# Kernel tuning notes

Hardware: AMD Instinct MI355X
Metric: run time of the kernel (lower is better)

## Reference

```python
import jax, jax.numpy as jnp
import numpy as np

B, H, N, D = 2, 16, 2048, 128

def setup_inputs() -> dict:
    key = jax.random.key(0)
    kq, kk, kv = jax.random.split(key, 3)
    q = jax.random.normal(kq, (B, H, N, D), dtype=jnp.float32)
    k = jax.random.normal(kk, (B, H, N, D), dtype=jnp.float32)
    v = jax.random.normal(kv, (B, H, N, D), dtype=jnp.float32)
    return {"q": q, "k": k, "v": v}

def reference(q, k, v):
    # scale = 1/sqrt(d) computed at forward time (scale=None in __init__)
    d = q.shape[-1]
    scale = 1.0 / jnp.sqrt(jnp.asarray(d, dtype=q.dtype))
    # scores: (B, H, N, N)
    scores = jnp.einsum('bhnd,bhmd->bhnm', q, k) * scale
    probs = jax.nn.softmax(scores, axis=-1)
    return jnp.einsum('bhnm,bhmd->bhnd', probs, v)
```

## Files before the change

### kernel.cpp

```cpp
#include <hip/hip_runtime.h>
#include <hip/hip_fp16.h>

#define BH   32
#define SEQ  2048
#define DIM  128
#define CK   32
#define NCH  (SEQ / CK)

typedef _Float16 half8   __attribute__((ext_vector_type(8)));
typedef __fp16   fp16x2  __attribute__((ext_vector_type(2)));
typedef _Float16 half2v  __attribute__((ext_vector_type(2)));
typedef float    floatx4 __attribute__((ext_vector_type(4)));

__device__ inline half2v pk2(float a, float b) {
    fp16x2 t = __builtin_amdgcn_cvt_pkrtz(a, b);
    return *(half2v*)&t;
}
__device__ inline half8 pk8(float4 a, float4 b) {
    half2v l0 = pk2(a.x, a.y), l1 = pk2(a.z, a.w);
    half2v l2 = pk2(b.x, b.y), l3 = pk2(b.z, b.w);
    half8 h;
    h[0] = l0[0]; h[1] = l0[1]; h[2] = l1[0]; h[3] = l1[1];
    h[4] = l2[0]; h[5] = l2[1]; h[6] = l3[0]; h[7] = l3[1];
    return h;
}

__device__ inline void ld16(const void* g, void* l) {
    __builtin_amdgcn_global_load_lds(
        (__attribute__((address_space(1))) void*)(uintptr_t)g,
        (__attribute__((address_space(3))) void*)(uintptr_t)l, 16, 0, 0);
}

__device__ inline void wait_vm0() {
    __builtin_amdgcn_s_waitcnt(0x0F70);
}

__global__ void prep_kernel(const float* __restrict__ k, const float* __restrict__ v,
                            _Float16* __restrict__ kh, _Float16* __restrict__ vt) {
    const float SC = 0.08838834764831845f * 1.4426950408889634f;
    __shared__ __align__(16) _Float16 t[32][136];
    const int bh = blockIdx.x >> 6;
    const int kc = blockIdx.x & 63;
    const int tid = threadIdx.x;
    const size_t base = ((size_t)bh * SEQ + kc * CK) * DIM;

    const float4* kf4 = (const float4*)(k + base);
    const float4* vf4 = (const float4*)(v + base);
    half8* kh8 = (half8*)(kh + base);

    #pragma unroll
    for (int i = 0; i < 2; i++) {
        int f8 = i * 256 + tid;
        float4 a = kf4[2 * f8], b = kf4[2 * f8 + 1];
        a.x *= SC; a.y *= SC; a.z *= SC; a.w *= SC;
        b.x *= SC; b.y *= SC; b.z *= SC; b.w *= SC;
        kh8[f8] = pk8(a, b);
        int row = f8 >> 4, c8 = f8 & 15;
        *((half8*)&t[row][c8 * 8]) = pk8(vf4[2 * f8], vf4[2 * f8 + 1]);
    }
    __syncthreads();
    _Float16* vout = vt + ((size_t)bh * NCH + kc) * (DIM * CK);
    #pragma unroll
    for (int i = 0; i < 2; i++) {
        int g = i * 256 + tid;
        int d = g >> 2, kg = g & 3;
        half8 h;
        #pragma unroll
        for (int j = 0; j < 8; j++) h[j] = t[kg * 8 + j][d];
        *((half8*)(vout + d * CK + kg * 8)) = h;
    }
}

__global__ __launch_bounds__(256, 2) void attn_kernel(
        const float* __restrict__ q, const _Float16* __restrict__ kh,
        const _Float16* __restrict__ vt, float* __restrict__ out) {
    __shared__ __align__(16) _Float16 Kbuf[2][CK * DIM];
    __shared__ __align__(16) _Float16 Vbuf[2][DIM * CK];
    __shared__ __align__(16) _Float16 Pld[4][2][16][40];

    const int bh   = blockIdx.y;
    const int qt   = blockIdx.x;
    const int tid  = threadIdx.x;
    const int w    = tid >> 6;
    const int lane = tid & 63;
    const int l15  = lane & 15;
    const int quad = lane >> 4;

    half8 qf[2][4];
    #pragma unroll
    for (int s = 0; s < 2; s++) {
        const float* qb = q + ((size_t)bh * SEQ + qt * 128 + w * 32 + s * 16 + l15) * DIM;
        #pragma unroll
        for (int c = 0; c < 4; c++) {
            float4 a = *((const float4*)(qb + c * 32 + quad * 8));
            float4 b = *((const float4*)(qb + c * 32 + quad * 8 + 4));
            qf[s][c] = pk8(a, b);
        }
    }

    half8 ones;
    #pragma unroll
    for (int j = 0; j < 8; j++) ones[j] = (_Float16)1.0f;

    floatx4 zf = {0.f, 0.f, 0.f, 0.f};
    floatx4 O[2][8];
    #pragma unroll
    for (int s = 0; s < 2; s++)
        #pragma unroll
        for (int i = 0; i < 8; i++) O[s][i] = zf;
    floatx4 Osum[2] = {zf, zf};

    const _Float16* kb = kh + (size_t)bh * SEQ * DIM;
    const _Float16* vb = vt + (size_t)bh * SEQ * DIM;

    const int s0 = w * 128 + lane;
    const int s1 = s0 + 64;
    const int kr0 = s0 >> 4, kg0 = ((s0 & 15) - kr0) & 15;
    const int kr1 = s1 >> 4, kg1 = ((s1 & 15) - kr1) & 15;
    const _Float16* kgp0 = kb + kr0 * DIM + kg0 * 8;
    const _Float16* kgp1 = kb + kr1 * DIM + kg1 * 8;
    const _Float16* vgp0 = vb + s0 * 8;
    const _Float16* vgp1 = vb + s1 * 8;

    auto dma = [&](int kc, int b) {
        size_t off = (size_t)kc * (CK * DIM);
        ld16(kgp0 + off, &Kbuf[b][(w * 2 + 0) * 512]);
        ld16(kgp1 + off, &Kbuf[b][(w * 2 + 1) * 512]);
        ld16(vgp0 + off, &Vbuf[b][(w * 2 + 0) * 512]);
        ld16(vgp1 + off, &Vbuf[b][(w * 2 + 1) * 512]);
    };

    dma(0, 0);

    const int row0 = 2 * l15, row1 = 2 * l15 + 1;

    #pragma unroll 2
    for (int kc = 0; kc < NCH; kc++) {
        wait_vm0();
        __syncthreads();
        if (kc + 1 < NCH) dma(kc + 1, (kc + 1) & 1);

        const _Float16* Kc = Kbuf[kc & 1];
        const _Float16* Vc = Vbuf[kc & 1];

        floatx4 S[2][2];
        #pragma unroll
        for (int s = 0; s < 2; s++) { S[s][0] = zf; S[s][1] = zf; }
        #pragma unroll
        for (int c = 0; c < 4; c++) {
            int g = c * 4 + quad;
            half8 b0 = *((const half8*)&Kc[row0 * DIM + (((g + row0) & 15) * 8)]);
            half8 b1 = *((const half8*)&Kc[row1 * DIM + (((g + row1) & 15) * 8)]);
            #pragma unroll
            for (int s = 0; s < 2; s++) {
                S[s][0] = __builtin_amdgcn_mfma_f32_16x16x32_f16(qf[s][c], b0, S[s][0], 0, 0, 0);
                S[s][1] = __builtin_amdgcn_mfma_f32_16x16x32_f16(qf[s][c], b1, S[s][1], 0, 0, 0);
            }
        }

        #pragma unroll
        for (int s = 0; s < 2; s++)
            #pragma unroll
            for (int r = 0; r < 4; r++) {
                float p0 = exp2f(S[s][0][r]);
                float p1 = exp2f(S[s][1][r]);
                *((half2v*)&Pld[w][s][quad * 4 + r][2 * l15]) = pk2(p0, p1);
            }

        half8 pf0 = *((const half8*)&Pld[w][0][l15][quad * 8]);
        half8 pf1 = *((const half8*)&Pld[w][1][l15][quad * 8]);

        Osum[0] = __builtin_amdgcn_mfma_f32_16x16x32_f16(pf0, ones, Osum[0], 0, 0, 0);
        Osum[1] = __builtin_amdgcn_mfma_f32_16x16x32_f16(pf1, ones, Osum[1], 0, 0, 0);

        #pragma unroll
        for (int dt = 0; dt < 8; dt++) {
            half8 vf = *((const half8*)&Vc[(dt * 16 + l15) * CK + quad * 8]);
            O[0][dt] = __builtin_amdgcn_mfma_f32_16x16x32_f16(pf0, vf, O[0][dt], 0, 0, 0);
            O[1][dt] = __builtin_amdgcn_mfma_f32_16x16x32_f16(pf1, vf, O[1][dt], 0, 0, 0);
        }
    }

    #pragma unroll
    for (int s = 0; s < 2; s++) {
        float* ob = out + ((size_t)bh * SEQ + qt * 128 + w * 32 + s * 16) * DIM;
        #pragma unroll
        for (int r = 0; r < 4; r++) {
            float rinv = 1.0f / Osum[s][r];
            #pragma unroll
            for (int dt = 0; dt < 8; dt++) {
                ob[(size_t)(quad * 4 + r) * DIM + dt * 16 + l15] = O[s][dt][r] * rinv;
            }
        }
    }
}

extern "C" void kernel_launch(void* const* d_in, const int* in_sizes, int n_in,
                              void* d_out, int out_size, void* d_ws, size_t ws_size,
                              hipStream_t stream) {
    const float* q = (const float*)d_in[0];
    const float* k = (const float*)d_in[1];
    const float* v = (const float*)d_in[2];
    float* out = (float*)d_out;

    const size_t elems = (size_t)BH * SEQ * DIM;
    _Float16* kh = (_Float16*)d_ws;
    _Float16* vtp = kh + elems;

    prep_kernel<<<BH * NCH, 256, 0, stream>>>(k, v, kh, vtp);
    attn_kernel<<<dim3(SEQ / 128, BH), 256, 0, stream>>>(q, kh, vtp, out);
}
```

Measured before the change: 212.0 us.

## Triple-buffer K/V DMA with prefetch distance two and XCD-aware block remap

Widens the K/V LDS ring from two to three buffers and issues DMA two chunks ahead. The wait becomes a partial vmcnt(4) plus a single barrier, so the next chunk's loads stay in flight while the current one is computed. The block index is remapped so that blocks for the same batch-head land on the same XCD, which should improve L2 reuse of K/V. The change also hoists the V fragment reads ahead of the softmax step and raises wave priority around the MFMA sections. In exchange it uses more LDS per block and makes the waitcnt bookkeeping more delicate.

```diff
diff --git a/kernel.cpp b/kernel.cpp
--- a/kernel.cpp
+++ b/kernel.cpp
@@ -31,9 +31,11 @@
         (__attribute__((address_space(3))) void*)(uintptr_t)l, 16, 0, 0);
 }
 
-__device__ inline void wait_vm0() {
-    __builtin_amdgcn_s_waitcnt(0x0F70);
-}
+#define SYNC_VM(N) do {                                        \
+    asm volatile("s_waitcnt vmcnt(" #N ")" ::: "memory");      \
+    __builtin_amdgcn_s_barrier();                              \
+    asm volatile("" ::: "memory");                             \
+} while (0)
 
 __global__ void prep_kernel(const float* __restrict__ k, const float* __restrict__ v,
                             _Float16* __restrict__ kh, _Float16* __restrict__ vt) {
@@ -74,12 +76,16 @@
 __global__ __launch_bounds__(256, 2) void attn_kernel(
         const float* __restrict__ q, const _Float16* __restrict__ kh,
         const _Float16* __restrict__ vt, float* __restrict__ out) {
-    __shared__ __align__(16) _Float16 Kbuf[2][CK * DIM];
-    __shared__ __align__(16) _Float16 Vbuf[2][DIM * CK];
+    __shared__ __align__(16) _Float16 Kbuf[3][CK * DIM];
+    __shared__ __align__(16) _Float16 Vbuf[3][DIM * CK];
     __shared__ __align__(16) _Float16 Pld[4][2][16][40];
 
-    const int bh   = blockIdx.y;
-    const int qt   = blockIdx.x;
+    const int lid = blockIdx.x + (blockIdx.y << 4);
+    const int xcd = lid & 7;
+    const int idx = lid >> 3;
+    const int bh  = (xcd << 2) + (idx >> 4);
+    const int qt  = idx & 15;
+
     const int tid  = threadIdx.x;
     const int w    = tid >> 6;
     const int lane = tid & 63;
@@ -130,22 +136,16 @@
         ld16(vgp1 + off, &Vbuf[b][(w * 2 + 1) * 512]);
     };
 
-    dma(0, 0);
-
     const int row0 = 2 * l15, row1 = 2 * l15 + 1;
 
-    #pragma unroll 2
-    for (int kc = 0; kc < NCH; kc++) {
-        wait_vm0();
-        __syncthreads();
-        if (kc + 1 < NCH) dma(kc + 1, (kc + 1) & 1);
-
-        const _Float16* Kc = Kbuf[kc & 1];
-        const _Float16* Vc = Vbuf[kc & 1];
+    auto chunk = [&](int cb) {
+        const _Float16* Kc = Kbuf[cb];
+        const _Float16* Vc = Vbuf[cb];
 
         floatx4 S[2][2];
         #pragma unroll
         for (int s = 0; s < 2; s++) { S[s][0] = zf; S[s][1] = zf; }
+        __builtin_amdgcn_s_setprio(1);
         #pragma unroll
         for (int c = 0; c < 4; c++) {
             int g = c * 4 + quad;
@@ -157,6 +157,12 @@
                 S[s][1] = __builtin_amdgcn_mfma_f32_16x16x32_f16(qf[s][c], b1, S[s][1], 0, 0, 0);
             }
         }
+        __builtin_amdgcn_s_setprio(0);
+
+        half8 vfr[8];
+        #pragma unroll
+        for (int dt = 0; dt < 8; dt++)
+            vfr[dt] = *((const half8*)&Vc[(dt * 16 + l15) * CK + quad * 8]);
 
         #pragma unroll
         for (int s = 0; s < 2; s++)
@@ -170,16 +176,33 @@
         half8 pf0 = *((const half8*)&Pld[w][0][l15][quad * 8]);
         half8 pf1 = *((const half8*)&Pld[w][1][l15][quad * 8]);
 
+        __builtin_amdgcn_s_setprio(1);
         Osum[0] = __builtin_amdgcn_mfma_f32_16x16x32_f16(pf0, ones, Osum[0], 0, 0, 0);
         Osum[1] = __builtin_amdgcn_mfma_f32_16x16x32_f16(pf1, ones, Osum[1], 0, 0, 0);
-
         #pragma unroll
         for (int dt = 0; dt < 8; dt++) {
-            half8 vf = *((const half8*)&Vc[(dt * 16 + l15) * CK + quad * 8]);
-            O[0][dt] = __builtin_amdgcn_mfma_f32_16x16x32_f16(pf0, vf, O[0][dt], 0, 0, 0);
-            O[1][dt] = __builtin_amdgcn_mfma_f32_16x16x32_f16(pf1, vf, O[1][dt], 0, 0, 0);
-        }
-    }
+            O[0][dt] = __builtin_amdgcn_mfma_f32_16x16x32_f16(pf0, vfr[dt], O[0][dt], 0, 0, 0);
+            O[1][dt] = __builtin_amdgcn_mfma_f32_16x16x32_f16(pf1, vfr[dt], O[1][dt], 0, 0, 0);
+        }
+        __builtin_amdgcn_s_setprio(0);
+    };
+
+    dma(0, 0);
+    dma(1, 1);
+
+    int c0 = 0;
+    #pragma unroll 3
+    for (int kc = 0; kc < NCH - 1; kc++) {
+        SYNC_VM(4);
+        if (kc + 2 < NCH) {
+            int c2 = c0 + 2; if (c2 >= 3) c2 -= 3;
+            dma(kc + 2, c2);
+        }
+        chunk(c0);
+        c0 = (c0 == 2) ? 0 : c0 + 1;
+    }
+    SYNC_VM(0);
+    chunk(c0);
 
     #pragma unroll
     for (int s = 0; s < 2; s++) {
```

Result: no change. 214.0 us (+0.9%).
